# Kernel optimization log

Measured on AMD Instinct MI355X. Metric: run time of the kernel, lower is better.

## Reference

```python
import jax, jax.numpy as jnp
import numpy as np

B, W, F, H = 2048, 128, 8, 256
LN_EPS = 1e-5


def _gru_cell(h, xt, Wih, Whh, bih, bhh):
    # PyTorch GRU cell. Wih: [3H, Fin], Whh: [3H, H]
    gi = xt @ Wih.T + bih            # [B, 3H]
    gh = h @ Whh.T + bhh             # [B, 3H]
    ir, iz, inn = jnp.split(gi, 3, axis=-1)
    hr, hz, hn = jnp.split(gh, 3, axis=-1)
    r = jax.nn.sigmoid(ir + hr)
    z = jax.nn.sigmoid(iz + hz)
    n = jnp.tanh(inn + r * hn)
    return (1.0 - z) * n + z * h


def setup_inputs() -> dict:
    key = jax.random.key(0)
    ks = jax.random.split(key, 12)
    s = 1.0 / np.sqrt(H)   # torch GRU init: U(-1/sqrt(H), 1/sqrt(H))
    sp = 1.0 / np.sqrt(2 * H)  # torch Linear init fan_in = 2H
    u = lambda k, shp, sc: jax.random.uniform(k, shp, jnp.float32, -sc, sc)
    return {
        "x": jax.random.normal(ks[0], (B, W, F), jnp.float32),
        "Wih_f": u(ks[1], (3 * H, F), s), "Whh_f": u(ks[2], (3 * H, H), s),
        "bih_f": u(ks[3], (3 * H,), s), "bhh_f": u(ks[4], (3 * H,), s),
        "Wih_b": u(ks[5], (3 * H, F), s), "Whh_b": u(ks[6], (3 * H, H), s),
        "bih_b": u(ks[7], (3 * H,), s), "bhh_b": u(ks[8], (3 * H,), s),
        "Wp": u(ks[9], (H, 2 * H), sp), "bp": u(ks[10], (H,), sp),
        "gamma": jnp.ones((H,), jnp.float32), "beta": jnp.zeros((H,), jnp.float32),
    }


def reference(x, Wih_f, Whh_f, bih_f, bhh_f, Wih_b, Whh_b, bih_b, bhh_b, Wp, bp, gamma, beta):
    b = x.shape[0]
    h0 = jnp.zeros((b, H), x.dtype)
    xs = jnp.swapaxes(x, 0, 1)  # [W, B, F]
    # Forward direction: only the final hidden state is used (out[:, -1, :H]).
    h_fwd, _ = jax.lax.scan(
        lambda h, xt: (_gru_cell(h, xt, Wih_f, Whh_f, bih_f, bhh_f), None), h0, xs)
    # Backward direction output at the LAST time index is its FIRST step
    # (reversed scan starting from h0 on x[:, -1]).
    h_bwd = _gru_cell(h0, x[:, -1, :], Wih_b, Whh_b, bih_b, bhh_b)
    last = jnp.concatenate([h_fwd, h_bwd], axis=-1)  # [B, 2H]
    y = jax.nn.gelu(last @ Wp.T + bp, approximate=False)
    mu = jnp.mean(y, axis=-1, keepdims=True)
    var = jnp.var(y, axis=-1, keepdims=True)
    yn = (y - mu) * jax.lax.rsqrt(var + LN_EPS)
    return yn * gamma + beta  # dropout is identity in eval mode
```

## Files before the change

kernel.cpp:

```cpp
#include <hip/hip_runtime.h>
#include <hip/hip_bf16.h>

#define BDIM 2048
#define WDIM 128
#define FDIM 8
#define HDIM 256

typedef __bf16 b8 __attribute__((ext_vector_type(8)));
typedef __bf16 b4 __attribute__((ext_vector_type(4)));
typedef float f32x4 __attribute__((ext_vector_type(4)));

#define L2E  1.44269504088896f
#define L2E2 2.88539008177793f

#define OFF_RZ  0
#define OFF_N   262144
#define OFF_WIH 393216
#define OFF_WP  442368
#define OFF_XB  704512

#define SMEM_BYTES 147456

#define MFMA(a,b,c) __builtin_amdgcn_mfma_f32_16x16x32_bf16((a),(b),(c),0,0,0)

static __device__ __forceinline__ float sig_(float v) {
    return __builtin_amdgcn_rcpf(1.0f + __expf(-v));
}
static __device__ __forceinline__ float tanh_(float v) {
    return fmaf(-2.0f, __builtin_amdgcn_rcpf(1.0f + __expf(2.0f * v)), 1.0f);
}

__global__ void pack_kernel(const float* __restrict__ x,
                            const float* __restrict__ Wih_f,
                            const float* __restrict__ Whh_f,
                            const float* __restrict__ bih_f,
                            const float* __restrict__ bhh_f,
                            const float* __restrict__ Wp,
                            unsigned char* __restrict__ ws)
{
    int idx = blockIdx.x * 256 + threadIdx.x;
    if (idx < 16384) {
        int l = idx & 63, f = idx >> 6;
        int kt = f & 7, nt = (f >> 3) & 1, g = (f >> 4) & 1, w = f >> 5;
        int gch = g * HDIM + 32 * w + 16 * nt + (l & 15);
        int kb = kt * 32 + (l >> 4) * 8;
        b8 v;
        #pragma unroll
        for (int e = 0; e < 8; ++e) v[e] = (__bf16)(-L2E * Whh_f[gch * HDIM + kb + e]);
        ((b8*)(ws + OFF_RZ))[idx] = v;
    } else if (idx < 24576) {
        int j = idx - 16384;
        int l = j & 63, f = j >> 6;
        int kt = f & 7, nt = (f >> 3) & 1, w = f >> 4;
        int gch = 2 * HDIM + 32 * w + 16 * nt + (l & 15);
        int kb = kt * 32 + (l >> 4) * 8;
        b8 v;
        #pragma unroll
        for (int e = 0; e < 8; ++e) v[e] = (__bf16)(L2E2 * Whh_f[gch * HDIM + kb + e]);
        ((b8*)(ws + OFF_N))[j] = v;
    } else if (idx < 27648) {
        int j = idx - 24576;
        int l = j & 63, f = j >> 6;
        int nt = f & 1, q = f >> 1, g = q % 3, w = q / 3;
        int gch = g * HDIM + 32 * w + 16 * nt + (l & 15);
        int lq = l >> 4;
        float sc = (g == 2) ? L2E2 : -L2E;
        b8 v;
        #pragma unroll
        for (int e = 0; e < 8; ++e) v[e] = (__bf16)0.0f;
        if (lq == 0) {
            #pragma unroll
            for (int e = 0; e < 8; ++e) v[e] = (__bf16)(sc * Wih_f[gch * FDIM + e]);
        } else if (lq == 1) {
            float b = (g == 2) ? (L2E2 * bih_f[gch]) : (-L2E * (bih_f[gch] + bhh_f[gch]));
            v[0] = (__bf16)b;
        }
        ((b8*)(ws + OFF_WIH))[j] = v;
    } else if (idx < 44032) {
        int j = idx - 27648;
        int l = j & 63, nk = j >> 6;
        int NT = nk >> 4, kt = nk & 15;
        int col = NT * 16 + (l & 15);
        int kb = kt * 32 + (l >> 4) * 8;
        b8 v;
        #pragma unroll
        for (int e = 0; e < 8; ++e) v[e] = (__bf16)Wp[col * (2 * HDIM) + kb + e];
        ((b8*)(ws + OFF_WP))[j] = v;
    } else if (idx < 44032 + 262144) {
        int j = idx - 44032;
        const float* src = x + j * 8;
        b8 v;
        #pragma unroll
        for (int e = 0; e < 8; ++e) v[e] = (__bf16)src[e];
        ((b8*)(ws + OFF_XB))[j] = v;
    }
}

__global__ __launch_bounds__(512, 2)
void gru_main_kernel(const float* __restrict__ x,
                     const float* __restrict__ bhh_f,
                     const float* __restrict__ Wih_b, const float* __restrict__ bih_b,
                     const float* __restrict__ bhh_b,
                     const float* __restrict__ bp,
                     const float* __restrict__ gamma, const float* __restrict__ beta,
                     const unsigned char* __restrict__ ws,
                     float* __restrict__ out)
{
    extern __shared__ __align__(16) unsigned char smem[];
    __bf16* hbB = (__bf16*)smem;
    b8* nlds = (b8*)(smem + 16384);
    __bf16 (*lastb)[2 * HDIM] = (__bf16(*)[2 * HDIM])smem;
    float  (*ybuf)[HDIM]      = (float(*)[HDIM])(smem + 16384);

    const int tid = threadIdx.x, lane = tid & 63, w = tid >> 6;
    const int l15 = lane & 15, lq = lane >> 4;
    const int blockRow = blockIdx.x * 16;

    const b8* wsRZ = (const b8*)(ws + OFF_RZ);
    const b8* wsN  = (const b8*)(ws + OFF_N);
    const b8* wsWI = (const b8*)(ws + OFF_WIH);
    const b8* wsWP = (const b8*)(ws + OFF_WP);
    const b8* xB   = (const b8*)(ws + OFF_XB);

    const f32x4 zero4 = {0.f, 0.f, 0.f, 0.f};

    *(f32x4*)(smem + tid * 16) = zero4;
    *(f32x4*)(smem + 8192 + tid * 16) = zero4;

    {
        const b8* nsrc = wsN + (w * 16) * 64 + lane;
        b8* ndst = nlds + (w * 16) * 64 + lane;
        #pragma unroll
        for (int i = 0; i < 16; ++i) ndst[i * 64] = nsrc[i * 64];
    }

    b8 whr[2][8], whz[2][8], wir[2], wiz[2], win[2];
    #pragma unroll
    for (int nt = 0; nt < 2; ++nt) {
        #pragma unroll
        for (int kt = 0; kt < 8; ++kt) {
            whr[nt][kt] = wsRZ[((w * 4 + 0 + nt) * 8 + kt) * 64 + lane];
            whz[nt][kt] = wsRZ[((w * 4 + 2 + nt) * 8 + kt) * 64 + lane];
        }
        wir[nt] = wsWI[((w * 3 + 0) * 2 + nt) * 64 + lane];
        wiz[nt] = wsWI[((w * 3 + 1) * 2 + nt) * 64 + lane];
        win[nt] = wsWI[((w * 3 + 2) * 2 + nt) * 64 + lane];
    }
    #pragma unroll
    for (int nt = 0; nt < 2; ++nt) {
        #pragma unroll
        for (int kt = 0; kt < 8; ++kt) {
            asm volatile("" : "+v"(whr[nt][kt]));
            asm volatile("" : "+v"(whz[nt][kt]));
        }
        asm volatile("" : "+v"(wir[nt]));
        asm volatile("" : "+v"(wiz[nt]));
        asm volatile("" : "+v"(win[nt]));
    }

    float4 t0v = *(const float4*)&bhh_f[2 * HDIM + 32 * w + 0  + 4 * lq];
    float4 t1v = *(const float4*)&bhh_f[2 * HDIM + 32 * w + 16 + 4 * lq];
    f32x4 bnv0, bnv1;
    bnv0[0] = L2E2 * t0v.x; bnv0[1] = L2E2 * t0v.y; bnv0[2] = L2E2 * t0v.z; bnv0[3] = L2E2 * t0v.w;
    bnv1[0] = L2E2 * t1v.x; bnv1[1] = L2E2 * t1v.y; bnv1[2] = L2E2 * t1v.z; bnv1[3] = L2E2 * t1v.w;

    b8 xc;
    #pragma unroll
    for (int e = 0; e < 8; ++e) xc[e] = (__bf16)0.0f;
    if (lq == 1) xc[0] = (__bf16)1.0f;

    f32x4 h0 = zero4, h1 = zero4;

    const int kswz = (8 * lq) ^ ((l15 & 7) << 3);
    const int wswz = (l15 & 7) << 3;
    const b8* nW = nlds + (w * 16) * 64 + lane;
    const b8* xRow = xB + (blockRow + l15) * WDIM;

    b8 xf = xc;
    if (lane < 16) xf = xRow[0];

    __syncthreads();

    int cur = 0;
    for (int t = 0; t < WDIM; ++t) {
        b8 xn = xc;
        if (lane < 16) xn = xRow[(t + 1) & 127];

        f32x4 aR0 = MFMA(wir[0], xf, zero4);
        f32x4 aR1 = MFMA(wir[1], xf, zero4);
        f32x4 aZ0 = MFMA(wiz[0], xf, zero4);
        f32x4 aZ1 = MFMA(wiz[1], xf, zero4);
        f32x4 aNX0 = MFMA(win[0], xf, zero4);
        f32x4 aNX1 = MFMA(win[1], xf, zero4);
        f32x4 aNH0 = bnv0, aNH1 = bnv1;

        const __bf16* hc = hbB + cur * 4096 + l15 * 256;
        #pragma unroll
        for (int kt = 0; kt < 8; ++kt) {
            b8 hfrag = *(const b8*)(hc + ((kt << 5) ^ kswz));
            b8 n0 = nW[kt * 64];
            b8 n1 = nW[(8 + kt) * 64];
            aR0  = MFMA(whr[0][kt], hfrag, aR0);
            aR1  = MFMA(whr[1][kt], hfrag, aR1);
            aZ0  = MFMA(whz[0][kt], hfrag, aZ0);
            aZ1  = MFMA(whz[1][kt], hfrag, aZ1);
            aNH0 = MFMA(n0, hfrag, aNH0);
            aNH1 = MFMA(n1, hfrag, aNH1);
        }

        __bf16* hn = hbB + (cur ^ 1) * 4096;
        b4 v0, v1;
        #pragma unroll
        for (int j = 0; j < 4; ++j) {
            float r = __builtin_amdgcn_rcpf(1.0f + __builtin_amdgcn_exp2f(aR0[j]));
            float z = __builtin_amdgcn_rcpf(1.0f + __builtin_amdgcn_exp2f(aZ0[j]));
            float u = fmaf(r, aNH0[j], aNX0[j]);
            float n = fmaf(-2.0f, __builtin_amdgcn_rcpf(1.0f + __builtin_amdgcn_exp2f(u)), 1.0f);
            float hv = n + z * (h0[j] - n);
            h0[j] = hv; v0[j] = (__bf16)hv;

            r = __builtin_amdgcn_rcpf(1.0f + __builtin_amdgcn_exp2f(aR1[j]));
            z = __builtin_amdgcn_rcpf(1.0f + __builtin_amdgcn_exp2f(aZ1[j]));
            u = fmaf(r, aNH1[j], aNX1[j]);
            n = fmaf(-2.0f, __builtin_amdgcn_rcpf(1.0f + __builtin_amdgcn_exp2f(u)), 1.0f);
            hv = n + z * (h1[j] - n);
            h1[j] = hv; v1[j] = (__bf16)hv;
        }
        *(b4*)(hn + l15 * 256 + ((32 * w + 0  + 4 * lq) ^ wswz)) = v0;
        *(b4*)(hn + l15 * 256 + ((32 * w + 16 + 4 * lq) ^ wswz)) = v1;

        xf = xn;
        cur ^= 1;
        __syncthreads();
    }

    {
        b4 v0, v1;
        #pragma unroll
        for (int j = 0; j < 4; ++j) { v0[j] = (__bf16)h0[j]; v1[j] = (__bf16)h1[j]; }
        *(b4*)(&lastb[l15][0] + ((32 * w + 0  + 4 * lq) ^ wswz)) = v0;
        *(b4*)(&lastb[l15][0] + ((32 * w + 16 + 4 * lq) ^ wswz)) = v1;
    }

    {
        const int trow = tid >> 5;
        const int cb = tid & 31;
        const float4* xr = (const float4*)(x + (blockRow + trow) * WDIM * FDIM + 127 * FDIM);
        float4 xv0 = xr[0], xv1 = xr[1];
        const float4* wb = (const float4*)Wih_b;
        #pragma unroll
        for (int jj = 0; jj < 8; ++jj) {
            int ch = cb + 32 * jj;
            float4 a0 = wb[ch * 2],               a1 = wb[ch * 2 + 1];
            float4 b0 = wb[(HDIM + ch) * 2],      b1 = wb[(HDIM + ch) * 2 + 1];
            float4 c0v = wb[(2 * HDIM + ch) * 2], c1 = wb[(2 * HDIM + ch) * 2 + 1];
            float ir = bih_b[ch]
                + xv0.x * a0.x + xv0.y * a0.y + xv0.z * a0.z + xv0.w * a0.w
                + xv1.x * a1.x + xv1.y * a1.y + xv1.z * a1.z + xv1.w * a1.w;
            float iz = bih_b[HDIM + ch]
                + xv0.x * b0.x + xv0.y * b0.y + xv0.z * b0.z + xv0.w * b0.w
                + xv1.x * b1.x + xv1.y * b1.y + xv1.z * b1.z + xv1.w * b1.w;
            float inn = bih_b[2 * HDIM + ch]
                + xv0.x * c0v.x + xv0.y * c0v.y + xv0.z * c0v.z + xv0.w * c0v.w
                + xv1.x * c1.x + xv1.y * c1.y + xv1.z * c1.z + xv1.w * c1.w;
            float r = sig_(ir + bhh_b[ch]);
            float z = sig_(iz + bhh_b[HDIM + ch]);
            float n = tanh_(fmaf(r, bhh_b[2 * HDIM + ch], inn));
            float hbw = (1.0f - z) * n;
            int c2 = HDIM + ch;
            lastb[trow][c2 ^ ((trow & 7) << 3)] = (__bf16)hbw;
        }
    }
    __syncthreads();

    {
        f32x4 pacc[2];
        #pragma unroll
        for (int nt = 0; nt < 2; ++nt) {
            int col = 32 * w + nt * 16 + l15;
            float b = bp[col];
            pacc[nt][0] = b; pacc[nt][1] = b; pacc[nt][2] = b; pacc[nt][3] = b;
        }
        #pragma unroll
        for (int kt = 0; kt < 16; ++kt) {
            int c = (kt * 32 + lq * 8) ^ ((l15 & 7) << 3);
            b8 a = *(const b8*)&lastb[l15][c];
            #pragma unroll
            for (int nt = 0; nt < 2; ++nt)
                pacc[nt] = MFMA(a, wsWP[((2 * w + nt) * 16 + kt) * 64 + lane], pacc[nt]);
        }
        #pragma unroll
        for (int nt = 0; nt < 2; ++nt) {
            int col = 32 * w + nt * 16 + l15;
            #pragma unroll
            for (int j = 0; j < 4; ++j) {
                int row = lq * 4 + j;
                float v = pacc[nt][j];
                ybuf[row][col] = 0.5f * v * (1.0f + erff(v * 0.70710678118f));
            }
        }
    }
    __syncthreads();

    #pragma unroll
    for (int rr = 0; rr < 2; ++rr) {
        int row = 2 * w + rr;
        float v[4];
        float s = 0.0f, sq = 0.0f;
        #pragma unroll
        for (int m = 0; m < 4; ++m) {
            v[m] = ybuf[row][lane + 64 * m];
            s += v[m];
            sq += v[m] * v[m];
        }
        #pragma unroll
        for (int off = 32; off >= 1; off >>= 1) {
            s  += __shfl_xor(s, off, 64);
            sq += __shfl_xor(sq, off, 64);
        }
        float mu = s * (1.0f / 256.0f);
        float var = sq * (1.0f / 256.0f) - mu * mu;
        float rs = rsqrtf(var + 1e-5f);
        float* orow = out + (blockRow + row) * HDIM;
        #pragma unroll
        for (int m = 0; m < 4; ++m) {
            int cc = lane + 64 * m;
            orow[cc] = (v[m] - mu) * rs * gamma[cc] + beta[cc];
        }
    }
}

extern "C" void kernel_launch(void* const* d_in, const int* in_sizes, int n_in,
                              void* d_out, int out_size, void* d_ws, size_t ws_size,
                              hipStream_t stream)
{
    const float* x     = (const float*)d_in[0];
    const float* Wih_f = (const float*)d_in[1];
    const float* Whh_f = (const float*)d_in[2];
    const float* bih_f = (const float*)d_in[3];
    const float* bhh_f = (const float*)d_in[4];
    const float* Wih_b = (const float*)d_in[5];
    const float* bih_b = (const float*)d_in[7];
    const float* bhh_b = (const float*)d_in[8];
    const float* Wp    = (const float*)d_in[9];
    const float* bp    = (const float*)d_in[10];
    const float* gamma = (const float*)d_in[11];
    const float* beta  = (const float*)d_in[12];
    float* out = (float*)d_out;
    unsigned char* ws = (unsigned char*)d_ws;

    hipFuncSetAttribute((const void*)gru_main_kernel,
                        hipFuncAttributeMaxDynamicSharedMemorySize, SMEM_BYTES);

    const int packItems = 16384 + 8192 + 3072 + 16384 + 262144;
    hipLaunchKernelGGL(pack_kernel, dim3((packItems + 255) / 256), dim3(256), 0, stream,
                       x, Wih_f, Whh_f, bih_f, bhh_f, Wp, ws);
    hipLaunchKernelGGL(gru_main_kernel, dim3(BDIM / 16), dim3(512), SMEM_BYTES, stream,
                       x, bhh_f, Wih_b, bih_b, bhh_b, bp, gamma, beta, ws, out);
}
```

Measured before the change: 196.7 us.

## Compute GRU r/z gates with FP8 MFMA and keep n-gate weights in registers

Measured after the change: 217.0 us. 1.1x slower.

```diff
diff --git a/kernel.cpp b/kernel.cpp
--- a/kernel.cpp
+++ b/kernel.cpp
@@ -9,25 +9,40 @@
 typedef __bf16 b8 __attribute__((ext_vector_type(8)));
 typedef __bf16 b4 __attribute__((ext_vector_type(4)));
 typedef float f32x4 __attribute__((ext_vector_type(4)));
+typedef long l64;
 
 #define L2E  1.44269504088896f
 #define L2E2 2.88539008177793f
 
-#define OFF_RZ  0
-#define OFF_N   262144
-#define OFF_WIH 393216
-#define OFF_WP  442368
-#define OFF_XB  704512
-
-#define SMEM_BYTES 147456
-
-#define MFMA(a,b,c) __builtin_amdgcn_mfma_f32_16x16x32_bf16((a),(b),(c),0,0,0)
+#define OFF_RZ8 0
+#define OFF_NB  131072
+#define OFF_WI8 262144
+#define OFF_WIN 278528
+#define OFF_WP  294912
+#define OFF_XB  557056
+
+#define MFMA(a,b,c)  __builtin_amdgcn_mfma_f32_16x16x32_bf16((a),(b),(c),0,0,0)
+#define MFMA8(a,b,c) __builtin_amdgcn_mfma_f32_16x16x32_fp8_fp8((a),(b),(c),0,0,0)
 
 static __device__ __forceinline__ float sig_(float v) {
     return __builtin_amdgcn_rcpf(1.0f + __expf(-v));
 }
 static __device__ __forceinline__ float tanh_(float v) {
     return fmaf(-2.0f, __builtin_amdgcn_rcpf(1.0f + __expf(2.0f * v)), 1.0f);
+}
+
+static __device__ __forceinline__ l64 pk8(const float* v) {
+    int lo = __builtin_amdgcn_cvt_pk_fp8_f32(v[0], v[1], 0, false);
+    lo = __builtin_amdgcn_cvt_pk_fp8_f32(v[2], v[3], lo, true);
+    int hi = __builtin_amdgcn_cvt_pk_fp8_f32(v[4], v[5], 0, false);
+    hi = __builtin_amdgcn_cvt_pk_fp8_f32(v[6], v[7], hi, true);
+    return ((l64)(unsigned)hi << 32) | (unsigned)lo;
+}
+static __device__ __forceinline__ l64 b8_to_f8(b8 v) {
+    float f[8];
+    #pragma unroll
+    for (int e = 0; e < 8; ++e) f[e] = (float)v[e];
+    return pk8(f);
 }
 
 __global__ void pack_kernel(const float* __restrict__ x,
@@ -44,10 +59,10 @@
         int kt = f & 7, nt = (f >> 3) & 1, g = (f >> 4) & 1, w = f >> 5;
         int gch = g * HDIM + 32 * w + 16 * nt + (l & 15);
         int kb = kt * 32 + (l >> 4) * 8;
-        b8 v;
-        #pragma unroll
-        for (int e = 0; e < 8; ++e) v[e] = (__bf16)(-L2E * Whh_f[gch * HDIM + kb + e]);
-        ((b8*)(ws + OFF_RZ))[idx] = v;
+        float v[8];
+        #pragma unroll
+        for (int e = 0; e < 8; ++e) v[e] = -L2E * Whh_f[gch * HDIM + kb + e];
+        ((l64*)(ws + OFF_RZ8))[idx] = pk8(v);
     } else if (idx < 24576) {
         int j = idx - 16384;
         int l = j & 63, f = j >> 6;
@@ -57,25 +72,39 @@
         b8 v;
         #pragma unroll
         for (int e = 0; e < 8; ++e) v[e] = (__bf16)(L2E2 * Whh_f[gch * HDIM + kb + e]);
-        ((b8*)(ws + OFF_N))[j] = v;
-    } else if (idx < 27648) {
+        ((b8*)(ws + OFF_NB))[j] = v;
+    } else if (idx < 26624) {
         int j = idx - 24576;
         int l = j & 63, f = j >> 6;
-        int nt = f & 1, q = f >> 1, g = q % 3, w = q / 3;
+        int nt = f & 1, g = (f >> 1) & 1, w = f >> 2;
         int gch = g * HDIM + 32 * w + 16 * nt + (l & 15);
         int lq = l >> 4;
-        float sc = (g == 2) ? L2E2 : -L2E;
+        float v[8];
+        #pragma unroll
+        for (int e = 0; e < 8; ++e) v[e] = 0.0f;
+        if (lq == 0) {
+            #pragma unroll
+            for (int e = 0; e < 8; ++e) v[e] = -L2E * Wih_f[gch * FDIM + e];
+        } else if (lq == 1) {
+            v[0] = -L2E * (bih_f[gch] + bhh_f[gch]);
+        }
+        ((l64*)(ws + OFF_WI8))[j] = pk8(v);
+    } else if (idx < 27648) {
+        int j = idx - 26624;
+        int l = j & 63, f = j >> 6;
+        int nt = f & 1, w = f >> 1;
+        int gch = 2 * HDIM + 32 * w + 16 * nt + (l & 15);
+        int lq = l >> 4;
         b8 v;
         #pragma unroll
         for (int e = 0; e < 8; ++e) v[e] = (__bf16)0.0f;
         if (lq == 0) {
             #pragma unroll
-            for (int e = 0; e < 8; ++e) v[e] = (__bf16)(sc * Wih_f[gch * FDIM + e]);
+            for (int e = 0; e < 8; ++e) v[e] = (__bf16)(L2E2 * Wih_f[gch * FDIM + e]);
         } else if (lq == 1) {
-            float b = (g == 2) ? (L2E2 * bih_f[gch]) : (-L2E * (bih_f[gch] + bhh_f[gch]));
-            v[0] = (__bf16)b;
-        }
-        ((b8*)(ws + OFF_WIH))[j] = v;
+            v[0] = (__bf16)(L2E2 * bih_f[gch]);
+        }
+        ((b8*)(ws + OFF_WIN))[j] = v;
     } else if (idx < 44032) {
         int j = idx - 27648;
         int l = j & 63, nk = j >> 6;
@@ -106,9 +135,9 @@
                      const unsigned char* __restrict__ ws,
                      float* __restrict__ out)
 {
-    extern __shared__ __align__(16) unsigned char smem[];
+    __shared__ __align__(16) unsigned char smem[32768];
     __bf16* hbB = (__bf16*)smem;
-    b8* nlds = (b8*)(smem + 16384);
+    unsigned char* hb8 = smem + 16384;
     __bf16 (*lastb)[2 * HDIM] = (__bf16(*)[2 * HDIM])smem;
     float  (*ybuf)[HDIM]      = (float(*)[HDIM])(smem + 16384);
 
@@ -116,46 +145,44 @@
     const int l15 = lane & 15, lq = lane >> 4;
     const int blockRow = blockIdx.x * 16;
 
-    const b8* wsRZ = (const b8*)(ws + OFF_RZ);
-    const b8* wsN  = (const b8*)(ws + OFF_N);
-    const b8* wsWI = (const b8*)(ws + OFF_WIH);
-    const b8* wsWP = (const b8*)(ws + OFF_WP);
-    const b8* xB   = (const b8*)(ws + OFF_XB);
+    const l64* wsRZ8 = (const l64*)(ws + OFF_RZ8);
+    const b8*  wsNB  = (const b8*)(ws + OFF_NB);
+    const l64* wsWI8 = (const l64*)(ws + OFF_WI8);
+    const b8*  wsWIN = (const b8*)(ws + OFF_WIN);
+    const b8*  wsWP  = (const b8*)(ws + OFF_WP);
+    const b8*  xB    = (const b8*)(ws + OFF_XB);
 
     const f32x4 zero4 = {0.f, 0.f, 0.f, 0.f};
 
     *(f32x4*)(smem + tid * 16) = zero4;
     *(f32x4*)(smem + 8192 + tid * 16) = zero4;
-
-    {
-        const b8* nsrc = wsN + (w * 16) * 64 + lane;
-        b8* ndst = nlds + (w * 16) * 64 + lane;
-        #pragma unroll
-        for (int i = 0; i < 16; ++i) ndst[i * 64] = nsrc[i * 64];
-    }
-
-    b8 whr[2][8], whz[2][8], wir[2], wiz[2], win[2];
+    *(f32x4*)(smem + 16384 + tid * 16) = zero4;
+
+    l64 whr8[2][8], whz8[2][8], wir8[2], wiz8[2];
+    b8 wnnB[2][8], winB[2];
     #pragma unroll
     for (int nt = 0; nt < 2; ++nt) {
         #pragma unroll
         for (int kt = 0; kt < 8; ++kt) {
-            whr[nt][kt] = wsRZ[((w * 4 + 0 + nt) * 8 + kt) * 64 + lane];
-            whz[nt][kt] = wsRZ[((w * 4 + 2 + nt) * 8 + kt) * 64 + lane];
-        }
-        wir[nt] = wsWI[((w * 3 + 0) * 2 + nt) * 64 + lane];
-        wiz[nt] = wsWI[((w * 3 + 1) * 2 + nt) * 64 + lane];
-        win[nt] = wsWI[((w * 3 + 2) * 2 + nt) * 64 + lane];
+            whr8[nt][kt] = wsRZ8[((w * 4 + 0 + nt) * 8 + kt) * 64 + lane];
+            whz8[nt][kt] = wsRZ8[((w * 4 + 2 + nt) * 8 + kt) * 64 + lane];
+            wnnB[nt][kt] = wsNB[((w * 2 + nt) * 8 + kt) * 64 + lane];
+        }
+        wir8[nt] = wsWI8[(w * 4 + 0 + nt) * 64 + lane];
+        wiz8[nt] = wsWI8[(w * 4 + 2 + nt) * 64 + lane];
+        winB[nt] = wsWIN[(w * 2 + nt) * 64 + lane];
     }
     #pragma unroll
     for (int nt = 0; nt < 2; ++nt) {
         #pragma unroll
         for (int kt = 0; kt < 8; ++kt) {
-            asm volatile("" : "+v"(whr[nt][kt]));
-            asm volatile("" : "+v"(whz[nt][kt]));
-        }
-        asm volatile("" : "+v"(wir[nt]));
-        asm volatile("" : "+v"(wiz[nt]));
-        asm volatile("" : "+v"(win[nt]));
+            asm volatile("" : "+v"(whr8[nt][kt]));
+            asm volatile("" : "+v"(whz8[nt][kt]));
+            asm volatile("" : "+a"(wnnB[nt][kt]));
+        }
+        asm volatile("" : "+v"(wir8[nt]));
+        asm volatile("" : "+v"(wiz8[nt]));
+        asm volatile("" : "+v"(winB[nt]));
     }
 
     float4 t0v = *(const float4*)&bhh_f[2 * HDIM + 32 * w + 0  + 4 * lq];
@@ -173,7 +200,6 @@
 
     const int kswz = (8 * lq) ^ ((l15 & 7) << 3);
     const int wswz = (l15 & 7) << 3;
-    const b8* nW = nlds + (w * 16) * 64 + lane;
     const b8* xRow = xB + (blockRow + l15) * WDIM;
 
     b8 xf = xc;
@@ -186,30 +212,34 @@
         b8 xn = xc;
         if (lane < 16) xn = xRow[(t + 1) & 127];
 
-        f32x4 aR0 = MFMA(wir[0], xf, zero4);
-        f32x4 aR1 = MFMA(wir[1], xf, zero4);
-        f32x4 aZ0 = MFMA(wiz[0], xf, zero4);
-        f32x4 aZ1 = MFMA(wiz[1], xf, zero4);
-        f32x4 aNX0 = MFMA(win[0], xf, zero4);
-        f32x4 aNX1 = MFMA(win[1], xf, zero4);
+        l64 xf8 = b8_to_f8(xf);
+
+        f32x4 aR0 = MFMA8(wir8[0], xf8, zero4);
+        f32x4 aR1 = MFMA8(wir8[1], xf8, zero4);
+        f32x4 aZ0 = MFMA8(wiz8[0], xf8, zero4);
+        f32x4 aZ1 = MFMA8(wiz8[1], xf8, zero4);
+        f32x4 aNX0 = MFMA(winB[0], xf, zero4);
+        f32x4 aNX1 = MFMA(winB[1], xf, zero4);
         f32x4 aNH0 = bnv0, aNH1 = bnv1;
 
-        const __bf16* hc = hbB + cur * 4096 + l15 * 256;
+        const __bf16* hcB = hbB + cur * 4096 + l15 * 256;
+        const unsigned char* hc8 = hb8 + cur * 4096 + l15 * 256;
         #pragma unroll
         for (int kt = 0; kt < 8; ++kt) {
-            b8 hfrag = *(const b8*)(hc + ((kt << 5) ^ kswz));
-            b8 n0 = nW[kt * 64];
-            b8 n1 = nW[(8 + kt) * 64];
-            aR0  = MFMA(whr[0][kt], hfrag, aR0);
-            aR1  = MFMA(whr[1][kt], hfrag, aR1);
-            aZ0  = MFMA(whz[0][kt], hfrag, aZ0);
-            aZ1  = MFMA(whz[1][kt], hfrag, aZ1);
-            aNH0 = MFMA(n0, hfrag, aNH0);
-            aNH1 = MFMA(n1, hfrag, aNH1);
-        }
-
-        __bf16* hn = hbB + (cur ^ 1) * 4096;
+            b8 hfB  = *(const b8*)(hcB + ((kt << 5) ^ kswz));
+            l64 hf8 = *(const l64*)(hc8 + ((kt << 5) ^ kswz));
+            aR0  = MFMA8(whr8[0][kt], hf8, aR0);
+            aR1  = MFMA8(whr8[1][kt], hf8, aR1);
+            aZ0  = MFMA8(whz8[0][kt], hf8, aZ0);
+            aZ1  = MFMA8(whz8[1][kt], hf8, aZ1);
+            aNH0 = MFMA(wnnB[0][kt], hfB, aNH0);
+            aNH1 = MFMA(wnnB[1][kt], hfB, aNH1);
+        }
+
+        __bf16* hnB = hbB + (cur ^ 1) * 4096;
+        unsigned char* hn8 = hb8 + (cur ^ 1) * 4096 + l15 * 256;
         b4 v0, v1;
+        float hv0[4], hv1[4];
         #pragma unroll
         for (int j = 0; j < 4; ++j) {
             float r = __builtin_amdgcn_rcpf(1.0f + __builtin_amdgcn_exp2f(aR0[j]));
@@ -217,17 +247,23 @@
             float u = fmaf(r, aNH0[j], aNX0[j]);
             float n = fmaf(-2.0f, __builtin_amdgcn_rcpf(1.0f + __builtin_amdgcn_exp2f(u)), 1.0f);
             float hv = n + z * (h0[j] - n);
-            h0[j] = hv; v0[j] = (__bf16)hv;
+            h0[j] = hv; v0[j] = (__bf16)hv; hv0[j] = hv;
 
             r = __builtin_amdgcn_rcpf(1.0f + __builtin_amdgcn_exp2f(aR1[j]));
             z = __builtin_amdgcn_rcpf(1.0f + __builtin_amdgcn_exp2f(aZ1[j]));
             u = fmaf(r, aNH1[j], aNX1[j]);
             n = fmaf(-2.0f, __builtin_amdgcn_rcpf(1.0f + __builtin_amdgcn_exp2f(u)), 1.0f);
             hv = n + z * (h1[j] - n);
-            h1[j] = hv; v1[j] = (__bf16)hv;
-        }
-        *(b4*)(hn + l15 * 256 + ((32 * w + 0  + 4 * lq) ^ wswz)) = v0;
-        *(b4*)(hn + l15 * 256 + ((32 * w + 16 + 4 * lq) ^ wswz)) = v1;
+            h1[j] = hv; v1[j] = (__bf16)hv; hv1[j] = hv;
+        }
+        *(b4*)(hnB + l15 * 256 + ((32 * w + 0  + 4 * lq) ^ wswz)) = v0;
+        *(b4*)(hnB + l15 * 256 + ((32 * w + 16 + 4 * lq) ^ wswz)) = v1;
+        int p0 = __builtin_amdgcn_cvt_pk_fp8_f32(hv0[0], hv0[1], 0, false);
+        p0 = __builtin_amdgcn_cvt_pk_fp8_f32(hv0[2], hv0[3], p0, true);
+        int p1 = __builtin_amdgcn_cvt_pk_fp8_f32(hv1[0], hv1[1], 0, false);
+        p1 = __builtin_amdgcn_cvt_pk_fp8_f32(hv1[2], hv1[3], p1, true);
+        *(int*)(hn8 + ((32 * w + 0  + 4 * lq) ^ wswz)) = p0;
+        *(int*)(hn8 + ((32 * w + 16 + 4 * lq) ^ wswz)) = p1;
 
         xf = xn;
         cur ^= 1;
@@ -349,12 +385,9 @@
     float* out = (float*)d_out;
     unsigned char* ws = (unsigned char*)d_ws;
 
-    hipFuncSetAttribute((const void*)gru_main_kernel,
-                        hipFuncAttributeMaxDynamicSharedMemorySize, SMEM_BYTES);
-
-    const int packItems = 16384 + 8192 + 3072 + 16384 + 262144;
+    const int packItems = 16384 + 8192 + 2048 + 1024 + 16384 + 262144;
     hipLaunchKernelGGL(pack_kernel, dim3((packItems + 255) / 256), dim3(256), 0, stream,
                        x, Wih_f, Whh_f, bih_f, bhh_f, Wp, ws);
-    hipLaunchKernelGGL(gru_main_kernel, dim3(BDIM / 16), dim3(512), SMEM_BYTES, stream,
+    hipLaunchKernelGGL(gru_main_kernel, dim3(BDIM / 16), dim3(512), 0, stream,
                        x, bhh_f, Wih_b, bih_b, bhh_b, bp, gamma, beta, ws, out);
 }
```
